# Optimization experiments

Measured on AMD Instinct MI355X. Metric: run time of the kernel, lower is better.

The kernel has to match this reference:

```python
import jax, jax.numpy as jnp
import numpy as np

N, T, L = 4, 2048, 2048
DQIN, DFEAT, DQK, DV = 32, 34, 64, 64  # modality feat=34 -> V input = 34-2 = 32, K input = last col


def _sorted_timeline(k, shape):
    return jnp.sort(jax.random.uniform(k, shape, jnp.float32) * 100.0, axis=-1)


def setup_inputs() -> dict:
    key = jax.random.key(0)
    ks = jax.random.split(key, 32)
    inp = {}
    inp["ref_data"] = jax.random.normal(ks[0], (N, 1, T, DQIN), jnp.float32)
    inp["ref_t"] = _sorted_timeline(ks[1], (N, 1, T))
    inp["m1_data"] = jax.random.normal(ks[2], (N, 1, L, DFEAT), jnp.float32)
    inp["m1_t"] = _sorted_timeline(ks[3], (N, 1, L))
    inp["m2_data"] = jax.random.normal(ks[4], (N, 1, L, DFEAT), jnp.float32)
    inp["m2_t"] = _sorted_timeline(ks[5], (N, 1, L))
    inp["m3_data"] = jax.random.normal(ks[6], (N, 1, L, DFEAT), jnp.float32)
    inp["m3_t"] = _sorted_timeline(ks[7], (N, 1, L))
    # shared W_Q (bias=False): d_q_in -> d_qk
    inp["Wq"] = jax.random.normal(ks[8], (DQIN, DQK), jnp.float32) / np.sqrt(DQIN)
    # per-modality params: W_K: 1 -> d_qk (with bias), W_V: (DFEAT-2) -> d_v (with bias), log-temperature
    for i, m in enumerate(["1", "2", "3"]):
        b = 9 + 4 * i
        inp["Wk" + m] = jax.random.normal(ks[b], (1, DQK), jnp.float32)
        inp["bk" + m] = jax.random.normal(ks[b + 1], (DQK,), jnp.float32) * 0.02
        inp["Wv" + m] = jax.random.normal(ks[b + 2], (DFEAT - 2, DV), jnp.float32) / np.sqrt(DFEAT - 2)
        inp["bv" + m] = jax.random.normal(ks[b + 3], (DV,), jnp.float32) * 0.02
        inp["log_tau" + m] = jnp.zeros((), jnp.float32)  # log(init_tau=1)
    return inp


def _unimodal(Q, ref_t, data, t, Wk, bk, Wv, bv, log_tau):
    # K path: last feature column through linear, then feature_map_k = [1, -x]
    Kr = data[..., -1:] @ Wk + bk                                   # (N,1,L,DQK)
    K = jnp.concatenate([jnp.ones(Kr.shape[:-1] + (1,), Kr.dtype), -Kr], axis=-1)  # (N,1,L,DQK+1)
    V = data[..., :-2] @ Wv + bv                                    # (N,1,L,DV)
    tau = jnp.exp(log_tau)
    # gaussian weight: -(Q.K)^2 / tau
    S = -jnp.square(jnp.einsum('nhtc,nhlc->nhtl', Q, K)) / tau       # (N,1,T,L)
    mask = (ref_t[..., :, None] >= t[..., None, :]).astype(S.dtype)  # (N,1,T,L)
    A = jax.nn.softmax(S * mask, axis=-1) * mask
    return jnp.einsum('nhtl,nhlc->nhtc', A, V)                       # (N,1,T,DV)


def reference(ref_data, ref_t, m1_data, m1_t, m2_data, m2_t, m3_data, m3_t,
              Wq, Wk1, bk1, Wv1, bv1, log_tau1, Wk2, bk2, Wv2, bv2, log_tau2,
              Wk3, bk3, Wv3, bv3, log_tau3):
    # compute_Q (qk_type='time'): Q = add_one(W_Q(ref_data)) -> append ones column
    Qr = jnp.einsum('nhtd,dk->nhtk', ref_data, Wq)
    Q = jnp.concatenate([Qr, jnp.ones(Qr.shape[:-1] + (1,), Qr.dtype)], axis=-1)  # (N,1,T,DQK+1)
    y1 = _unimodal(Q, ref_t, m1_data, m1_t, Wk1, bk1, Wv1, bv1, log_tau1)
    y2 = _unimodal(Q, ref_t, m2_data, m2_t, Wk2, bk2, Wv2, bv2, log_tau2)
    y3 = _unimodal(Q, ref_t, m3_data, m3_t, Wk3, bk3, Wv3, bv3, log_tau3)
    # original returns dict {m1: y1, m2: y2, m3: y3}; stacked here (3,N,1,T,DV)
    return jnp.stack([y1, y2, y3], axis=0)
```

## Files before the change

kernel.cpp:

```cpp
#include <hip/hip_runtime.h>

namespace {

typedef unsigned int uint;
typedef unsigned short ushort_t;
typedef __attribute__((ext_vector_type(8))) short bf16x8;
typedef __attribute__((ext_vector_type(4))) float f32x4;

constexpr int N = 4, T = 2048, L = 2048;
constexpr int DQIN = 32, DQK = 64;

constexpr int VI_SZ = 3 * N * 64 * L;
constexpr int X_SZ = 3 * N * L;
constexpr int A_SZ = 3 * N * T;

union PK8 { int i[4]; bf16x8 s; };

__global__ __launch_bounds__(256) void mm_prep(
    const float* __restrict__ ref_data, const float* __restrict__ ref_t,
    const float* __restrict__ d1, const float* __restrict__ t1,
    const float* __restrict__ d2, const float* __restrict__ t2,
    const float* __restrict__ d3, const float* __restrict__ t3,
    const float* __restrict__ Wq,
    const float* __restrict__ Wk1, const float* __restrict__ bk1,
    const float* __restrict__ Wv1, const float* __restrict__ bv1, const float* __restrict__ lt1,
    const float* __restrict__ Wk2, const float* __restrict__ bk2,
    const float* __restrict__ Wv2, const float* __restrict__ bv2, const float* __restrict__ lt2,
    const float* __restrict__ Wk3, const float* __restrict__ bk3,
    const float* __restrict__ Wv3, const float* __restrict__ bv3, const float* __restrict__ lt3,
    float* __restrict__ Aq, float* __restrict__ Gq, int* __restrict__ Cq,
    ushort_t* __restrict__ VI, float* __restrict__ X) {
  const int b = blockIdx.x;
  const int tid = threadIdx.x;

  if (b < 96) {
    const int m = b >> 5;
    const int idx = (b & 31) * 256 + tid;
    __shared__ float sWq[DQIN * DQK];
    __shared__ float sWk[DQK];
    __shared__ float sbk[DQK];
    const float* Wk = (m == 0) ? Wk1 : (m == 1 ? Wk2 : Wk3);
    const float* bk = (m == 0) ? bk1 : (m == 1 ? bk2 : bk3);
    const float* lt = (m == 0) ? lt1 : (m == 1 ? lt2 : lt3);
    for (int i = tid; i < DQIN * DQK; i += 256) sWq[i] = Wq[i];
    if (tid < DQK) { sWk[tid] = Wk[tid]; sbk[tid] = bk[tid]; }
    __syncthreads();
    float x[DQIN];
    const float* rp = ref_data + idx * DQIN;
#pragma unroll
    for (int i = 0; i < DQIN; i++) x[i] = rp[i];
    float qr[DQK];
#pragma unroll
    for (int j = 0; j < DQK; j += 4) {
      float4 acc4 = make_float4(0.f, 0.f, 0.f, 0.f);
#pragma unroll
      for (int i = 0; i < DQIN; i++) {
        const float4 w = *(const float4*)&sWq[i * DQK + j];
        acc4.x = fmaf(x[i], w.x, acc4.x);
        acc4.y = fmaf(x[i], w.y, acc4.y);
        acc4.z = fmaf(x[i], w.z, acc4.z);
        acc4.w = fmaf(x[i], w.w, acc4.w);
      }
      qr[j] = acc4.x; qr[j + 1] = acc4.y; qr[j + 2] = acc4.z; qr[j + 3] = acc4.w;
    }
    const float rs = __expf(-0.5f * lt[0]);
    float g = 0.f, h = 0.f;
#pragma unroll
    for (int j = 1; j < DQK; j++) {
      g = fmaf(qr[j], sWk[j - 1], g);
      h = fmaf(qr[j], sbk[j - 1], h);
    }
    g += sWk[DQK - 1];
    h += sbk[DQK - 1];
    Aq[m * (N * T) + idx] = (qr[0] - h) * rs;
    Gq[m * (N * T) + idx] = g * rs;
  } else if (b < 192) {
    const int sidx = (b - 96) * 256 + tid;
    const int m = sidx >> 13;
    const int nt = sidx & 8191;
    const int n = nt >> 11;
    const float rt = ref_t[nt];
    const float* tml = ((m == 0) ? t1 : (m == 1 ? t2 : t3)) + n * L;
    int lo = 0, hi = L;
    while (lo < hi) {
      const int mid = (lo + hi) >> 1;
      if (tml[mid] <= rt) lo = mid + 1; else hi = mid;
    }
    Cq[m * 8192 + nt] = lo;
  } else {
    const int vb = b - 192;
    const int mn = vb >> 5;
    const int m = mn >> 2, n = mn & 3;
    const int lseg0 = (vb & 31) * 64;
    const float* dm = (m == 0) ? d1 : (m == 1 ? d2 : d3);
    const float* Wv = (m == 0) ? Wv1 : (m == 1 ? Wv2 : Wv3);
    const float* bv = (m == 0) ? bv1 : (m == 1 ? bv2 : bv3);
    const int cdim = tid & 63;
    const int qq = tid >> 6;
    const int l0 = lseg0 + qq * 16;

    float Wc[32];
#pragma unroll
    for (int i = 0; i < 32; i++) Wc[i] = Wv[i * 64 + cdim];
    const float bvc = bv[cdim];

    uint hi16[16], lo16[16];
#pragma unroll 4
    for (int k = 0; k < 16; k++) {
      const float* dp = dm + (size_t)(n * L + l0 + k) * 34;
      float acc = bvc;
#pragma unroll
      for (int i = 0; i < 32; i++) acc = fmaf(dp[i], Wc[i], acc);
      uint u = __float_as_uint(acc);
      uint h = (u + 0x7fffu + ((u >> 16) & 1u)) & 0xffff0000u;
      float res = acc - __uint_as_float(h);
      uint ul = __float_as_uint(res);
      uint hl = (ul + 0x7fffu + ((ul >> 16) & 1u)) >> 16;
      hi16[k] = h >> 16;
      lo16[k] = hl;
    }
    int pkh[8], pkl[8];
#pragma unroll
    for (int p = 0; p < 8; p++) {
      pkh[p] = (int)(hi16[2 * p] | (hi16[2 * p + 1] << 16));
      pkl[p] = (int)(lo16[2 * p] | (lo16[2 * p + 1] << 16));
    }
    ushort_t* dst = VI + (size_t)(mn * 64 + cdim) * (2 * L) + (l0 >> 3) * 16;
    *(int4*)dst = make_int4(pkh[0], pkh[1], pkh[2], pkh[3]);
    *(int4*)(dst + 8) = make_int4(pkl[0], pkl[1], pkl[2], pkl[3]);
    *(int4*)(dst + 16) = make_int4(pkh[4], pkh[5], pkh[6], pkh[7]);
    *(int4*)(dst + 24) = make_int4(pkl[4], pkl[5], pkl[6], pkl[7]);

    if (tid < 64) {
      const int l = lseg0 + tid;
      X[mn * L + l] = dm[(size_t)(n * L + l) * 34 + 33];
    }
  }
}

__device__ inline void stage_chunk(ushort_t* dstbuf, const ushort_t* VIb, int ch,
                                   int w, int lane) {
#pragma unroll
  for (int i = 0; i < 8; i++) {
    const int u = w * 512 + i * 64 + lane;
    const int rr = u >> 4;
    const int gs = u & 15;
    const int g = (gs - rr) & 15;
    const ushort_t* src = VIb + (size_t)rr * 4096 + ch * 128 + g * 8;
    __builtin_amdgcn_global_load_lds(
        (const __attribute__((address_space(1))) void*)src,
        (__attribute__((address_space(3))) void*)(dstbuf + (size_t)(w * 512 + i * 64) * 8),
        16, 0, 0);
  }
}

__global__ __launch_bounds__(128) void mm_attn_main(
    const ushort_t* __restrict__ VI, const float* __restrict__ X,
    const float* __restrict__ Aq, const float* __restrict__ Gq, const int* __restrict__ Cq,
    float* __restrict__ out) {
  __shared__ ushort_t sbuf[2][8192];

  const int b = blockIdx.x;
  const int mn = b % 12;
  const int k = b / 12;

  const int tid = threadIdx.x;
  const int lane = tid & 63;
  const int w = tid >> 6;
  const int q = lane >> 4;
  const int m16 = lane & 15;

  const int rg = (w == 0) ? k : (127 - k);
  const int tbase = mn * T + rg * 16;

  const int c = Cq[tbase + m16];
  const int cmax = __shfl(c, 15, 64);
  const int cmin = __shfl(c, 0, 64);
  const int nch = (cmax + 63) >> 6;

  const int cB = Cq[mn * T + (127 - k) * 16 + 15];
  const int nchB = (cB + 63) >> 6;

  const float a = Aq[tbase + m16];
  const float g = Gq[tbase + m16];

  f32x4 acc[4];
#pragma unroll
  for (int ct = 0; ct < 4; ct++) acc[ct] = (f32x4){0.f, 0.f, 0.f, 0.f};
  float z = 0.f;

  const ushort_t* VIb = VI + (size_t)mn * 64 * 4096;
  const float* xp = X + mn * L;

  stage_chunk(sbuf[0], VIb, 0, w, lane);
  __syncthreads();

  for (int ch = 0; ch < nchB; ch++) {
    const int nb = ch & 1;
    if (ch + 1 < nchB) stage_chunk(sbuf[nb ^ 1], VIb, ch + 1, w, lane);

    if (ch < nch) {
      const int base = ch << 6;
      const ushort_t* buf = sbuf[nb];
      const bool inter = (base + 64 <= cmin);
#pragma unroll
      for (int kk = 0; kk < 2; kk++) {
        const int k0 = base + kk * 32 + q * 8;
        const float4 xa = *(const float4*)&xp[k0];
        const float4 xb = *(const float4*)&xp[k0 + 4];
        const float xs[8] = {xa.x, xa.y, xa.z, xa.w, xb.x, xb.y, xb.z, xb.w};
        float wv[8];
        if (inter) {
#pragma unroll
          for (int j = 0; j < 8; j++) {
            const float d = fmaf(-g, xs[j], a);
            wv[j] = __expf(-d * d);
            z += wv[j];
          }
        } else {
#pragma unroll
          for (int j = 0; j < 8; j++) {
            const float d = fmaf(-g, xs[j], a);
            const float e = __expf(-d * d);
            wv[j] = (k0 + j < c) ? e : 0.f;
            z += wv[j];
          }
        }
        PK8 ph, pl;
#pragma unroll
        for (int p2 = 0; p2 < 4; p2++) {
          const uint u0 = __float_as_uint(wv[2 * p2]);
          const uint u1 = __float_as_uint(wv[2 * p2 + 1]);
          const uint h0 = u0 & 0xffff0000u, h1 = u1 & 0xffff0000u;
          const float l0f = wv[2 * p2] - __uint_as_float(h0);
          const float l1f = wv[2 * p2 + 1] - __uint_as_float(h1);
          ph.i[p2] = (int)((h0 >> 16) | h1);
          pl.i[p2] = (int)((__float_as_uint(l0f) >> 16) | (__float_as_uint(l1f) & 0xffff0000u));
        }
        const bf16x8 ahi = ph.s, alo = pl.s;
#pragma unroll
        for (int ct = 0; ct < 4; ct++) {
          const int r = ct * 16 + m16;
          const int go = (kk * 4 + q) * 2;
          const int uih = r * 16 + ((go + r) & 15);
          const int uil = r * 16 + ((go + 1 + r) & 15);
          const bf16x8 bh = *(const bf16x8*)&buf[(size_t)uih * 8];
          const bf16x8 bl = *(const bf16x8*)&buf[(size_t)uil * 8];
          acc[ct] = __builtin_amdgcn_mfma_f32_16x16x32_bf16(ahi, bh, acc[ct], 0, 0, 0);
          acc[ct] = __builtin_amdgcn_mfma_f32_16x16x32_bf16(ahi, bl, acc[ct], 0, 0, 0);
          acc[ct] = __builtin_amdgcn_mfma_f32_16x16x32_bf16(alo, bh, acc[ct], 0, 0, 0);
        }
      }
    }
    __syncthreads();
  }

  z += __shfl_xor(z, 16, 64);
  z += __shfl_xor(z, 32, 64);

#pragma unroll
  for (int rr = 0; rr < 4; rr++) {
    const int row = q * 4 + rr;
    const float zr = __shfl(z, row, 64);
    const int cr = __shfl(c, row, 64);
    const float inv = 1.0f / (zr + (float)(L - cr));
#pragma unroll
    for (int ct = 0; ct < 4; ct++) {
      out[(size_t)(tbase + row) * 64 + ct * 16 + m16] = acc[ct][rr] * inv;
    }
  }
}

}

extern "C" void kernel_launch(void* const* d_in, const int* in_sizes, int n_in,
                              void* d_out, int out_size, void* d_ws, size_t ws_size,
                              hipStream_t stream) {
  const float* ref_data = (const float*)d_in[0];
  const float* ref_t = (const float*)d_in[1];
  const float* m1_data = (const float*)d_in[2];
  const float* m1_t = (const float*)d_in[3];
  const float* m2_data = (const float*)d_in[4];
  const float* m2_t = (const float*)d_in[5];
  const float* m3_data = (const float*)d_in[6];
  const float* m3_t = (const float*)d_in[7];
  const float* Wq = (const float*)d_in[8];
  const float* Wk1 = (const float*)d_in[9];
  const float* bk1 = (const float*)d_in[10];
  const float* Wv1 = (const float*)d_in[11];
  const float* bv1 = (const float*)d_in[12];
  const float* lt1 = (const float*)d_in[13];
  const float* Wk2 = (const float*)d_in[14];
  const float* bk2 = (const float*)d_in[15];
  const float* Wv2 = (const float*)d_in[16];
  const float* bv2 = (const float*)d_in[17];
  const float* lt2 = (const float*)d_in[18];
  const float* Wk3 = (const float*)d_in[19];
  const float* bk3 = (const float*)d_in[20];
  const float* Wv3 = (const float*)d_in[21];
  const float* bv3 = (const float*)d_in[22];
  const float* lt3 = (const float*)d_in[23];

  float* ws = (float*)d_ws;
  ushort_t* VI = (ushort_t*)ws;
  float* Xw = ws + VI_SZ;
  float* Aq = Xw + X_SZ;
  float* Gq = Aq + A_SZ;
  int* Cq = (int*)(Gq + A_SZ);

  mm_prep<<<dim3(576), dim3(256), 0, stream>>>(
      ref_data, ref_t, m1_data, m1_t, m2_data, m2_t, m3_data, m3_t, Wq,
      Wk1, bk1, Wv1, bv1, lt1, Wk2, bk2, Wv2, bv2, lt2, Wk3, bk3, Wv3, bv3, lt3,
      Aq, Gq, Cq, VI, Xw);
  mm_attn_main<<<dim3(12 * 64), dim3(128), 0, stream>>>(
      VI, Xw, Aq, Gq, Cq, (float*)d_out);
}
```

Before: 171.2 us.

## Split output dims across two blocks and stage X in shared memory

The main attention kernel now splits the 64 output columns into two halves handled by separate blocks, doubling the grid to 1536 blocks and halving per-block V staging and accumulators. The full X row is preloaded into LDS with async global-to-LDS loads, LDS offsets are precomputed, and launch bounds request 3 blocks per CU. This raises parallelism and occupancy on a small grid, at the cost of recomputing the exp weights twice, once per half.

```diff
diff --git a/kernel.cpp b/kernel.cpp
--- a/kernel.cpp
+++ b/kernel.cpp
@@ -141,28 +141,31 @@
 __device__ inline void stage_chunk(ushort_t* dstbuf, const ushort_t* VIb, int ch,
                                    int w, int lane) {
 #pragma unroll
-  for (int i = 0; i < 8; i++) {
-    const int u = w * 512 + i * 64 + lane;
-    const int rr = u >> 4;
+  for (int i = 0; i < 4; i++) {
+    const int u = (w * 4 + i) * 64 + lane;
+    const int lr = u >> 4;
     const int gs = u & 15;
-    const int g = (gs - rr) & 15;
-    const ushort_t* src = VIb + (size_t)rr * 4096 + ch * 128 + g * 8;
+    const int g = (gs - lr) & 15;
+    const ushort_t* src = VIb + (size_t)lr * 4096 + ch * 128 + g * 8;
     __builtin_amdgcn_global_load_lds(
         (const __attribute__((address_space(1))) void*)src,
-        (__attribute__((address_space(3))) void*)(dstbuf + (size_t)(w * 512 + i * 64) * 8),
+        (__attribute__((address_space(3))) void*)(dstbuf + (w * 4 + i) * 512),
         16, 0, 0);
   }
 }
 
-__global__ __launch_bounds__(128) void mm_attn_main(
+__global__ __launch_bounds__(128, 3) void mm_attn_main(
     const ushort_t* __restrict__ VI, const float* __restrict__ X,
     const float* __restrict__ Aq, const float* __restrict__ Gq, const int* __restrict__ Cq,
     float* __restrict__ out) {
-  __shared__ ushort_t sbuf[2][8192];
+  __shared__ ushort_t sbuf[2][4096];
+  __shared__ float sx[2048];
 
   const int b = blockIdx.x;
   const int mn = b % 12;
-  const int k = b / 12;
+  const int r = b / 12;
+  const int k = r >> 1;
+  const int dh = r & 1;
 
   const int tid = threadIdx.x;
   const int lane = tid & 63;
@@ -184,14 +187,33 @@
   const float a = Aq[tbase + m16];
   const float g = Gq[tbase + m16];
 
-  f32x4 acc[4];
-#pragma unroll
-  for (int ct = 0; ct < 4; ct++) acc[ct] = (f32x4){0.f, 0.f, 0.f, 0.f};
+  f32x4 acc[2];
+  acc[0] = (f32x4){0.f, 0.f, 0.f, 0.f};
+  acc[1] = (f32x4){0.f, 0.f, 0.f, 0.f};
   float z = 0.f;
 
-  const ushort_t* VIb = VI + (size_t)mn * 64 * 4096;
-  const float* xp = X + mn * L;
-
+  const ushort_t* VIb = VI + (size_t)(mn * 64 + dh * 32) * 4096;
+  const float* xg = X + mn * L;
+
+  int oh[2][2], ol[2][2];
+#pragma unroll
+  for (int ct = 0; ct < 2; ct++) {
+#pragma unroll
+    for (int kk = 0; kk < 2; kk++) {
+      const int lr = ct * 16 + m16;
+      oh[ct][kk] = lr * 128 + (((kk * 8 + q * 2 + 0) + lr) & 15) * 8;
+      ol[ct][kk] = lr * 128 + (((kk * 8 + q * 2 + 1) + lr) & 15) * 8;
+    }
+  }
+
+#pragma unroll
+  for (int i = 0; i < 4; i++) {
+    const float* src = xg + (w * 4 + i) * 256 + lane * 4;
+    __builtin_amdgcn_global_load_lds(
+        (const __attribute__((address_space(1))) void*)src,
+        (__attribute__((address_space(3))) void*)(sx + (w * 4 + i) * 256),
+        16, 0, 0);
+  }
   stage_chunk(sbuf[0], VIb, 0, w, lane);
   __syncthreads();
 
@@ -206,8 +228,8 @@
 #pragma unroll
       for (int kk = 0; kk < 2; kk++) {
         const int k0 = base + kk * 32 + q * 8;
-        const float4 xa = *(const float4*)&xp[k0];
-        const float4 xb = *(const float4*)&xp[k0 + 4];
+        const float4 xa = *(const float4*)&sx[k0];
+        const float4 xb = *(const float4*)&sx[k0 + 4];
         const float xs[8] = {xa.x, xa.y, xa.z, xa.w, xb.x, xb.y, xb.z, xb.w};
         float wv[8];
         if (inter) {
@@ -239,13 +261,9 @@
         }
         const bf16x8 ahi = ph.s, alo = pl.s;
 #pragma unroll
-        for (int ct = 0; ct < 4; ct++) {
-          const int r = ct * 16 + m16;
-          const int go = (kk * 4 + q) * 2;
-          const int uih = r * 16 + ((go + r) & 15);
-          const int uil = r * 16 + ((go + 1 + r) & 15);
-          const bf16x8 bh = *(const bf16x8*)&buf[(size_t)uih * 8];
-          const bf16x8 bl = *(const bf16x8*)&buf[(size_t)uil * 8];
+        for (int ct = 0; ct < 2; ct++) {
+          const bf16x8 bh = *(const bf16x8*)(buf + oh[ct][kk]);
+          const bf16x8 bl = *(const bf16x8*)(buf + ol[ct][kk]);
           acc[ct] = __builtin_amdgcn_mfma_f32_16x16x32_bf16(ahi, bh, acc[ct], 0, 0, 0);
           acc[ct] = __builtin_amdgcn_mfma_f32_16x16x32_bf16(ahi, bl, acc[ct], 0, 0, 0);
           acc[ct] = __builtin_amdgcn_mfma_f32_16x16x32_bf16(alo, bh, acc[ct], 0, 0, 0);
@@ -265,8 +283,8 @@
     const int cr = __shfl(c, row, 64);
     const float inv = 1.0f / (zr + (float)(L - cr));
 #pragma unroll
-    for (int ct = 0; ct < 4; ct++) {
-      out[(size_t)(tbase + row) * 64 + ct * 16 + m16] = acc[ct][rr] * inv;
+    for (int ct = 0; ct < 2; ct++) {
+      out[(size_t)(tbase + row) * 64 + dh * 32 + ct * 16 + m16] = acc[ct][rr] * inv;
     }
   }
 }
@@ -312,6 +330,6 @@
       ref_data, ref_t, m1_data, m1_t, m2_data, m2_t, m3_data, m3_t, Wq,
       Wk1, bk1, Wv1, bv1, lt1, Wk2, bk2, Wv2, bv2, lt2, Wk3, bk3, Wv3, bv3, lt3,
       Aq, Gq, Cq, VI, Xw);
-  mm_attn_main<<<dim3(12 * 64), dim3(128), 0, stream>>>(
+  mm_attn_main<<<dim3(12 * 64 * 2), dim3(128), 0, stream>>>(
       VI, Xw, Aq, Gq, Cq, (float*)d_out);
 }
```

New measurement: 148.8 us. 1.15x faster.
